# Kernel tuning notes

Hardware: AMD Instinct MI355X
Metric: run time of the kernel (lower is better)

Reference implementation:

```python
import jax, jax.numpy as jnp
import numpy as np
import math

N = 4900      # hardcoded in source (hQ[708:4900])
N1 = 708      # hardcoded group-1 size
IN, OUT, HEADS = 512, 256, 4
HD = OUT // HEADS


def _ln(x, g, b, eps):
    mu = jnp.mean(x, axis=-1, keepdims=True)
    var = jnp.var(x, axis=-1, keepdims=True)
    return (x - mu) / jnp.sqrt(var + eps) * g + b


def setup_inputs() -> dict:
    key = jax.random.key(0)
    ks = jax.random.split(key, 24)
    s = 0.05
    nrm = lambda k, shp: jax.random.normal(k, shp, jnp.float32) * s
    return {
        "feature": jax.random.normal(ks[0], (N, IN), jnp.float32),
        "adj_mat": jax.random.uniform(ks[1], (N, N), jnp.float32),
        "r": jax.random.normal(ks[2], (4, 256), jnp.float32),
        "Wq": nrm(ks[3], (IN, OUT)), "bq": jnp.zeros((OUT,), jnp.float32),
        "Wk": nrm(ks[4], (IN, OUT)), "bk": jnp.zeros((OUT,), jnp.float32),
        "Wv": nrm(ks[5], (IN, OUT)), "bv": jnp.zeros((OUT,), jnp.float32),
        "Ww": nrm(ks[6], (IN, OUT)), "bw": jnp.zeros((OUT,), jnp.float32),
        "Wr": nrm(ks[7], (256, OUT)), "br": jnp.zeros((OUT,), jnp.float32),
        "Wbeta": nrm(ks[8], (2 * OUT, OUT)), "bbeta": jnp.zeros((OUT,), jnp.float32),
        "ln1_g": jnp.ones((OUT,), jnp.float32), "ln1_b": jnp.zeros((OUT,), jnp.float32),
        "w1": nrm(ks[9], (OUT, OUT)), "b1": jnp.zeros((OUT,), jnp.float32),
        "ln2_g": jnp.ones((OUT,), jnp.float32), "ln2_b": jnp.zeros((OUT,), jnp.float32),
        "w2": nrm(ks[10], (OUT, OUT)),
        "flag": 1,
    }


def reference(feature, adj_mat, r, Wq, bq, Wk, bk, Wv, bv, Ww, bw, Wr, br,
              Wbeta, bbeta, ln1_g, ln1_b, w1, b1, ln2_g, ln2_b, w2, flag):
    H = feature @ Ww + bw                     # [N, OUT]
    rp = r @ Wr + br                          # [4, OUT]
    hQ = feature @ Wq + bq
    hK = feature @ Wk + bk
    hV = (feature @ Wv + bv).reshape(HEADS, N, HD)  # raw block reshape, as in source
    ridx = 1 if flag else 0
    # relation-modulated Q/K blocks; .view == raw reshape in the original
    hQ11 = (hQ[:N1] * rp[ridx]).reshape(HEADS, N1, HD)
    hK11 = (hK[:N1] * rp[ridx]).reshape(HEADS, N1, HD)
    hQ12 = (hQ[:N1] * rp[2]).reshape(HEADS, N1, HD)
    hQ21 = (hQ[N1:] * rp[2]).reshape(HEADS, N - N1, HD)
    hQ22 = (hQ[N1:] * rp[3]).reshape(HEADS, N - N1, HD)
    hK12 = (hK[:N1] * rp[2]).reshape(HEADS, N1, HD)
    hK21 = (hK[N1:] * rp[2]).reshape(HEADS, N - N1, HD)
    hK22 = (hK[N1:] * rp[3]).reshape(HEADS, N - N1, HD)
    a11 = jnp.einsum('hqd,hkd->hqk', hQ11, hK11)
    a12 = jnp.einsum('hqd,hkd->hqk', hQ12, hK21)
    a21 = jnp.einsum('hqd,hkd->hqk', hQ21, hK12)
    a22 = jnp.einsum('hqd,hkd->hqk', hQ22, hK22)
    alpha = jnp.concatenate([jnp.concatenate([a11, a12], axis=2),
                             jnp.concatenate([a21, a22], axis=2)], axis=1)
    alpha = alpha / math.sqrt(HEADS)          # source divides by sqrt(heads)
    alpha = alpha @ adj_mat                   # [HEADS, N, N] @ [N, N]
    # torch nn.Softmax() legacy default dim for 3D input is dim=0
    alpha = jax.nn.softmax(alpha, axis=0)
    m = alpha @ hV                            # [HEADS, N, HD]
    m = jnp.transpose(m, (1, 0, 2)).reshape(N, OUT)
    m = _ln(jax.nn.relu(m), ln1_g, ln1_b, 1e-5)
    beta = jax.nn.sigmoid(jnp.concatenate([H, m], axis=1) @ Wbeta + bbeta)
    out = beta * m + (1.0 - beta) * H
    h = jnp.tanh(_ln(out @ w1 + b1, ln2_g, ln2_b, 1e-6))
    return h @ w2
```

## Files before the change

kernel.cpp:

```cpp
#include <hip/hip_runtime.h>
#include <hip/hip_bf16.h>
#include <math.h>

#define NPOS 4900
#define NG1  708
#define NG2  4192
#define INF  512
#define OUTF 256
#define JBP  4928
#define NJT  154
#define NC   6
#define JTT  26
#define LDS_KS 36
#define PCH   2508800
#define KSPL 2112

typedef __attribute__((ext_vector_type(8))) short short8;
typedef __attribute__((ext_vector_type(16))) float f32x16;

__global__ __launch_bounds__(256) void k0_rp(
    const float* __restrict__ r, const float* __restrict__ Wr,
    const float* __restrict__ br, const int* __restrict__ flagp,
    float* __restrict__ S)
{
    __shared__ float rsh[1024];
    int t = threadIdx.x;
    for (int i = t; i < 1024; i += 256) rsh[i] = r[i];
    __syncthreads();
    float a0 = 0.f, a1 = 0.f, a2 = 0.f, a3 = 0.f;
    for (int c = 0; c < 256; ++c) {
        float w = Wr[c * 256 + t];
        a0 += rsh[c] * w;
        a1 += rsh[256 + c] * w;
        a2 += rsh[512 + c] * w;
        a3 += rsh[768 + c] * w;
    }
    float b = br[t];
    a0 += b; a1 += b; a2 += b; a3 += b;
    int ridx = (flagp[0] != 0) ? 1 : 0;
    S[t]         = ridx ? a1 : a0;
    S[256 + t]   = a2;
    S[512 + t]   = a3;
}

__global__ __launch_bounds__(256) void k1_proj(
    const float* __restrict__ feat,
    const float* __restrict__ Wq, const float* __restrict__ bq,
    const float* __restrict__ Wk, const float* __restrict__ bk,
    const float* __restrict__ Wv, const float* __restrict__ bv,
    const float* __restrict__ Ww, const float* __restrict__ bw,
    float* __restrict__ hQ, float* __restrict__ hK,
    float* __restrict__ hV, float* __restrict__ Hb)
{
    __shared__ float AT[16][68];
    __shared__ float Bs[16][132];
    int t = threadIdx.x;
    int mat = blockIdx.x >> 1;
    int n0  = (blockIdx.x & 1) * 128;
    int m0  = blockIdx.y * 64;
    const float* W; const float* bias; float* dst;
    switch (mat) {
        case 0:  W = Wq; bias = bq; dst = hQ; break;
        case 1:  W = Wk; bias = bk; dst = hK; break;
        case 2:  W = Wv; bias = bv; dst = hV; break;
        default: W = Ww; bias = bw; dst = Hb; break;
    }
    float acc[4][8];
#pragma unroll
    for (int i = 0; i < 4; ++i)
#pragma unroll
        for (int j = 0; j < 8; ++j) acc[i][j] = 0.f;
    int mg = (t >> 4) * 4, jg = (t & 15) * 8;
    int am = t & 63, ak = (t >> 6) * 4;
    int bkk = t >> 4, bn = (t & 15) * 8;
    for (int k0 = 0; k0 < INF; k0 += 16) {
        __syncthreads();
        {
            int row = m0 + am;
            float4 v = make_float4(0.f, 0.f, 0.f, 0.f);
            if (row < NPOS) v = *(const float4*)(feat + (size_t)row * INF + k0 + ak);
            AT[ak + 0][am] = v.x; AT[ak + 1][am] = v.y;
            AT[ak + 2][am] = v.z; AT[ak + 3][am] = v.w;
        }
        {
            const float* p = W + (size_t)(k0 + bkk) * OUTF + n0 + bn;
            float4 u0 = *(const float4*)p;
            float4 u1 = *(const float4*)(p + 4);
            *(float4*)&Bs[bkk][bn]     = u0;
            *(float4*)&Bs[bkk][bn + 4] = u1;
        }
        __syncthreads();
#pragma unroll
        for (int kk = 0; kk < 16; ++kk) {
            float4 a  = *(const float4*)&AT[kk][mg];
            float4 b0 = *(const float4*)&Bs[kk][jg];
            float4 b1 = *(const float4*)&Bs[kk][jg + 4];
            float av[4] = {a.x, a.y, a.z, a.w};
            float bv_[8] = {b0.x, b0.y, b0.z, b0.w, b1.x, b1.y, b1.z, b1.w};
#pragma unroll
            for (int i = 0; i < 4; ++i)
#pragma unroll
                for (int j = 0; j < 8; ++j) acc[i][j] += av[i] * bv_[j];
        }
    }
#pragma unroll
    for (int i = 0; i < 4; ++i) {
        int row = m0 + mg + i;
        if (row < NPOS) {
#pragma unroll
            for (int j = 0; j < 8; ++j) {
                int n = n0 + jg + j;
                dst[(size_t)row * OUTF + n] = acc[i][j] + bias[n];
            }
        }
    }
}

__device__ __forceinline__ void split2(float x0, float x1,
                                       unsigned& hi, unsigned& lo)
{
    unsigned u0 = __float_as_uint(x0), u1 = __float_as_uint(x1);
    unsigned h0 = u0 & 0xFFFF0000u,   h1 = u1 & 0xFFFF0000u;
    float r0 = x0 - __uint_as_float(h0);
    float r1 = x1 - __uint_as_float(h1);
    hi = (h0 >> 16) | h1;
    lo = (__float_as_uint(r0) >> 16) | (__float_as_uint(r1) & 0xFFFF0000u);
}

__device__ __forceinline__ void split1(float x, unsigned short& hi, unsigned short& lo)
{
    unsigned u = __float_as_uint(x);
    unsigned h = u & 0xFFFF0000u;
    float r = x - __uint_as_float(h);
    hi = (unsigned short)(h >> 16);
    lo = (unsigned short)(__float_as_uint(r) >> 16);
}

__device__ __forceinline__ short8 ldfrag(const unsigned short* base, int row, int kuo)
{
    const unsigned long long* p =
        (const unsigned long long*)(base + row * LDS_KS + kuo);
    union { unsigned long long q[2]; short8 s; } u;
    u.q[0] = p[0];
    u.q[1] = p[1];
    return u.s;
}

__device__ __forceinline__ short8 g16(const unsigned short* p)
{
    union { uint4 q; short8 s; } u;
    u.q = *(const uint4*)p;
    return u.s;
}

__device__ __forceinline__ short8 lds16u(const unsigned short* p)
{
    union { unsigned long long q[2]; short8 s; } u;
    u.q[0] = ((const unsigned long long*)p)[0];
    u.q[1] = ((const unsigned long long*)p)[1];
    return u.s;
}

__global__ __launch_bounds__(256) void k2_mfma(
    const float* __restrict__ hK, const float* __restrict__ adj,
    const float* __restrict__ S,
    float* __restrict__ P0, float* __restrict__ P1)
{
    __shared__ unsigned short sAh[128 * LDS_KS];
    __shared__ unsigned short sAl[128 * LDS_KS];
    __shared__ unsigned short sBh[64 * LDS_KS];
    __shared__ unsigned short sBl[64 * LDS_KS];

    int t = threadIdx.x;
    int j0 = blockIdx.x * 64;
    int h  = blockIdx.y;
    int chunk = blockIdx.z;
    int part = (chunk == 0) ? 0 : 1;
    int kbeg = (chunk <= 1) ? 0 : KSPL;
    int kend = (chunk == 0) ? NG1 : ((chunk == 2) ? NG2 : KSPL);
    int L = part ? NG2 : NG1;
    const float* kflat = hK + (part ? (size_t)NG1 * OUTF : 0);
    int rowoff = part ? NG1 : 0;
    float* Pout = chunk ? (P1 + (size_t)(chunk - 1) * PCH) : P0;

    int dd = t & 63;
    int kg = t >> 6;
    int jcol = j0 + dd;

    float sc[2][4];
#pragma unroll
    for (int g = 0; g < 2; ++g)
#pragma unroll
        for (int c = 0; c < 4; ++c)
            sc[g][c] = 0.5f * S[(g + part) * 256 + c * 64 + dd];

    f32x16 acc0, acc1;
#pragma unroll
    for (int i = 0; i < 16; ++i) { acc0[i] = 0.f; acc1[i] = 0.f; }

    int lane = t & 63;
    int half = lane >> 5;
    int ml = lane & 31;
    int arow = kg * 32 + ml;

    unsigned* uAh = (unsigned*)sAh;
    unsigned* uAl = (unsigned*)sAl;
    unsigned* uBh = (unsigned*)sBh;
    unsigned* uBl = (unsigned*)sBl;

    int ks0 = kbeg >> 5;
    int ks1 = (kend + 31) >> 5;
    for (int ks = ks0; ks < ks1; ++ks) {
        int k0 = ks * 32;
        float xa[8], xb[8];
#pragma unroll
        for (int i = 0; i < 8; ++i) {
            int kv = k0 + kg * 8 + i;
            bool okk = (kv < kend);
            xa[i] = okk ? kflat[(size_t)(h * L + kv) * 64 + dd] : 0.f;
            xb[i] = (okk && jcol < NPOS)
                        ? adj[(size_t)(rowoff + kv) * NPOS + jcol] : 0.f;
        }
        unsigned hA0[4], lA0[4], hA1[4], lA1[4], hB[4], lB[4];
#pragma unroll
        for (int i = 0; i < 8; i += 2) {
            float a0 = xa[i] * sc[0][i & 3];
            float a1 = xa[i + 1] * sc[0][(i + 1) & 3];
            split2(a0, a1, hA0[i >> 1], lA0[i >> 1]);
            float c0 = xa[i] * sc[1][i & 3];
            float c1 = xa[i + 1] * sc[1][(i + 1) & 3];
            split2(c0, c1, hA1[i >> 1], lA1[i >> 1]);
            split2(xb[i], xb[i + 1], hB[i >> 1], lB[i >> 1]);
        }
        __syncthreads();
        {
            int b0 = dd * 18 + kg * 4;
            int b1 = (64 + dd) * 18 + kg * 4;
            *(uint2*)(uAh + b0)     = make_uint2(hA0[0], hA0[1]);
            *(uint2*)(uAh + b0 + 2) = make_uint2(hA0[2], hA0[3]);
            *(uint2*)(uAl + b0)     = make_uint2(lA0[0], lA0[1]);
            *(uint2*)(uAl + b0 + 2) = make_uint2(lA0[2], lA0[3]);
            *(uint2*)(uAh + b1)     = make_uint2(hA1[0], hA1[1]);
            *(uint2*)(uAh + b1 + 2) = make_uint2(hA1[2], hA1[3]);
            *(uint2*)(uAl + b1)     = make_uint2(lA1[0], lA1[1]);
            *(uint2*)(uAl + b1 + 2) = make_uint2(lA1[2], lA1[3]);
            *(uint2*)(uBh + b0)     = make_uint2(hB[0], hB[1]);
            *(uint2*)(uBh + b0 + 2) = make_uint2(hB[2], hB[3]);
            *(uint2*)(uBl + b0)     = make_uint2(lB[0], lB[1]);
            *(uint2*)(uBl + b0 + 2) = make_uint2(lB[2], lB[3]);
        }
        __syncthreads();
#pragma unroll
        for (int kq = 0; kq < 2; ++kq) {
            int kuo = kq * 16 + half * 8;
            short8 aH = ldfrag(sAh, arow, kuo);
            short8 aL = ldfrag(sAl, arow, kuo);
            short8 b0H = ldfrag(sBh, ml, kuo);
            short8 b0L = ldfrag(sBl, ml, kuo);
            short8 b1H = ldfrag(sBh, 32 + ml, kuo);
            short8 b1L = ldfrag(sBl, 32 + ml, kuo);
            acc0 = __builtin_amdgcn_mfma_f32_32x32x16_bf16(aH, b0H, acc0, 0, 0, 0);
            acc0 = __builtin_amdgcn_mfma_f32_32x32x16_bf16(aH, b0L, acc0, 0, 0, 0);
            acc0 = __builtin_amdgcn_mfma_f32_32x32x16_bf16(aL, b0H, acc0, 0, 0, 0);
            acc1 = __builtin_amdgcn_mfma_f32_32x32x16_bf16(aH, b1H, acc1, 0, 0, 0);
            acc1 = __builtin_amdgcn_mfma_f32_32x32x16_bf16(aH, b1L, acc1, 0, 0, 0);
            acc1 = __builtin_amdgcn_mfma_f32_32x32x16_bf16(aL, b1H, acc1, 0, 0, 0);
        }
    }

    int col0 = j0 + ml;
    int col1 = j0 + 32 + ml;
#pragma unroll
    for (int reg = 0; reg < 16; ++reg) {
        int m = kg * 32 + (reg & 3) + 8 * (reg >> 2) + 4 * half;
        int g = m >> 6, ddm = m & 63;
        size_t rb = (size_t)((h * 2 + g) * 64 + ddm) * NPOS;
        Pout[rb + col0] = acc0[reg];
        if (col1 < NPOS) Pout[rb + col1] = acc1[reg];
    }
}

__global__ __launch_bounds__(256) void k2_reduce(
    const float* __restrict__ P0, const float* __restrict__ P1,
    unsigned short* __restrict__ Bhi, unsigned short* __restrict__ Blo)
{
    int t = threadIdx.x;
    int j = blockIdx.x * 256 + t;
    if (j >= JBP) return;
    int p = blockIdx.y;
    int g = p >> 2, h = p & 3;
    int kg = blockIdx.z;
    int k0 = kg * 16;
    int rowb = (h * 2 + g) * 64;

    unsigned short hi[16], lo[16];
    if (j < NPOS) {
        if (k0 < 64) {
#pragma unroll
            for (int i = 0; i < 16; ++i) {
                float v = P0[(size_t)(rowb + k0 + i) * NPOS + j];
                split1(v, hi[i], lo[i]);
            }
        } else {
#pragma unroll
            for (int i = 0; i < 16; ++i) {
                size_t off = (size_t)(rowb + (k0 - 64) + i) * NPOS + j;
                float v = P1[off] + P1[off + PCH];
                split1(v, hi[i], lo[i]);
            }
        }
    } else {
#pragma unroll
        for (int i = 0; i < 16; ++i) { hi[i] = 0; lo[i] = 0; }
    }
    size_t base = ((size_t)p * JBP + j) * 128 + k0;
    union { unsigned short us[16]; uint4 v[2]; } uh, ul;
#pragma unroll
    for (int i = 0; i < 16; ++i) { uh.us[i] = hi[i]; ul.us[i] = lo[i]; }
    *(uint4*)(Bhi + base)     = uh.v[0];
    *(uint4*)(Bhi + base + 8) = uh.v[1];
    *(uint4*)(Blo + base)     = ul.v[0];
    *(uint4*)(Blo + base + 8) = ul.v[1];
}

__global__ __launch_bounds__(256) void qsplit(
    const float* __restrict__ hQ, const float* __restrict__ S,
    unsigned short* __restrict__ Qh, unsigned short* __restrict__ Ql)
{
    int t = threadIdx.x;
    int row = blockIdx.x * 2 + (t >> 7);
    int k = t & 127;
    int g, h, ql, Lg, vbase;
    if (row < 3072) { g = 0; h = row / 768; ql = row - h * 768; Lg = NG1; vbase = 0; }
    else {
        int rr = row - 3072;
        g = 1; h = rr / 4224; ql = rr - h * 4224; Lg = NG2; vbase = NG1 * OUTF;
    }
    int d = k & 63, p = k >> 6;
    float v = 0.f;
    if (ql < Lg)
        v = hQ[vbase + (size_t)(h * Lg + ql) * 64 + d] *
            S[(g + p) * 256 + (ql & 3) * 64 + d];
    unsigned short hi, lo;
    split1(v, hi, lo);
    Qh[(size_t)row * 128 + k] = hi;
    Ql[(size_t)row * 128 + k] = lo;
}

__global__ __launch_bounds__(256) void vtsplit(
    const float* __restrict__ hV,
    unsigned short* __restrict__ VtH, unsigned short* __restrict__ VtL)
{
    __shared__ float ls[128 * 65];
    int t = threadIdx.x;
    int j0 = blockIdx.x * 128;
    int h  = blockIdx.y;
#pragma unroll
    for (int i = 0; i < 32; ++i) {
        int idx = t + i * 256;
        int j = idx >> 6, d = idx & 63;
        float v = 0.f;
        int jg = j0 + j;
        if (jg < NPOS) v = hV[(size_t)(h * NPOS + jg) * 64 + d];
        ls[j * 65 + d] = v;
    }
    __syncthreads();
    int d = t >> 2, jseg = (t & 3) * 32;
#pragma unroll
    for (int i = 0; i < 32; ++i) {
        int j = jseg + i;
        int jg = j0 + j;
        if (jg < JBP) {
            unsigned short hi, lo;
            split1(ls[j * 65 + d], hi, lo);
            VtH[(size_t)(h * 64 + d) * JBP + jg] = hi;
            VtL[(size_t)(h * 64 + d) * JBP + jg] = lo;
        }
    }
}

__global__ __launch_bounds__(256, 2) void k3f_attn(
    const unsigned short* __restrict__ Qh, const unsigned short* __restrict__ Ql,
    const unsigned short* __restrict__ Bhi, const unsigned short* __restrict__ Blo,
    const unsigned short* __restrict__ VtH, const unsigned short* __restrict__ VtL,
    float* __restrict__ mpart)
{
    __shared__ __align__(16) char smem[35328];
    float* La = (float*)smem;
    unsigned short* Aa = (unsigned short*)(smem + 16896);

    int t = threadIdx.x;
    int w = t >> 6, lane = t & 63;
    int half = lane >> 5, ml = lane & 31;
    int h = w;

    int x = blockIdx.x;
    int c = blockIdx.y;
    int g = (x < 23) ? 0 : 1;
    int tile = g ? (x - 23) : x;
    int Lg = g ? NG2 : NG1;
    int posbase = g ? NG1 : 0;
    int qbase = g ? 3072 : 0;
    int hstr = g ? 4224 : 768;
    int q0 = tile * 32;

    const unsigned short* qrowH = Qh + (size_t)(qbase + h * hstr + q0 + ml) * 128 + half * 8;
    const unsigned short* qrowL = Ql + (size_t)(qbase + h * hstr + q0 + ml) * 128 + half * 8;
    short8 qfH[8], qfL[8];
#pragma unroll
    for (int kc = 0; kc < 8; ++kc) {
        qfH[kc] = g16(qrowH + kc * 16);
        qfL[kc] = g16(qrowL + kc * 16);
    }

    const unsigned short* bHb = Bhi + ((size_t)(g * 4 + h) * JBP + ml) * 128 + half * 8;
    const unsigned short* bLb = Blo + ((size_t)(g * 4 + h) * JBP + ml) * 128 + half * 8;
    size_t vro = (size_t)(h * 64 + ml) * JBP;
    const unsigned short* vH0 = VtH + vro;
    const unsigned short* vL0 = VtL + vro;
    const unsigned short* vH1 = VtH + vro + (size_t)32 * JBP;
    const unsigned short* vL1 = VtL + vro + (size_t)32 * JBP;

    f32x16 pv[2];
#pragma unroll
    for (int n = 0; n < 2; ++n)
#pragma unroll
        for (int r = 0; r < 16; ++r) pv[n][r] = 0.f;

    int spos = t >> 3, sj4 = (t & 7) * 4;

    int jt0 = c * JTT, jt1 = jt0 + JTT;
    if (jt1 > NJT) jt1 = NJT;

    for (int jt = jt0; jt < jt1; ++jt) {
        int j0 = jt * 32;
        const unsigned short* bH = bHb + (size_t)j0 * 128;
        const unsigned short* bL = bLb + (size_t)j0 * 128;

        short8 bb[8];
#pragma unroll
        for (int kc = 0; kc < 8; ++kc) bb[kc] = g16(bH + kc * 16);
        int joA = j0 + half * 8;
        int joB = j0 + 16 + half * 8;
        short8 vh0a = g16(vH0 + joA);
        short8 vh1a = g16(vH1 + joA);
        short8 vh0b = g16(vH0 + joB);
        short8 vh1b = g16(vH1 + joB);

        f32x16 qka, qkb;
#pragma unroll
        for (int r = 0; r < 16; ++r) { qka[r] = 0.f; qkb[r] = 0.f; }
#pragma unroll
        for (int kc = 0; kc < 8; kc += 2) {
            qka = __builtin_amdgcn_mfma_f32_32x32x16_bf16(bb[kc], qfH[kc], qka, 0, 0, 0);
            qka = __builtin_amdgcn_mfma_f32_32x32x16_bf16(bb[kc], qfL[kc], qka, 0, 0, 0);
            qkb = __builtin_amdgcn_mfma_f32_32x32x16_bf16(bb[kc + 1], qfH[kc + 1], qkb, 0, 0, 0);
            qkb = __builtin_amdgcn_mfma_f32_32x32x16_bf16(bb[kc + 1], qfL[kc + 1], qkb, 0, 0, 0);
        }
#pragma unroll
        for (int kc = 0; kc < 8; ++kc) bb[kc] = g16(bL + kc * 16);
#pragma unroll
        for (int kc = 0; kc < 8; kc += 2) {
            qka = __builtin_amdgcn_mfma_f32_32x32x16_bf16(bb[kc], qfH[kc], qka, 0, 0, 0);
            qkb = __builtin_amdgcn_mfma_f32_32x32x16_bf16(bb[kc + 1], qfH[kc + 1], qkb, 0, 0, 0);
        }

#pragma unroll
        for (int r = 0; r < 16; ++r) {
            int jrow = (r & 3) + 8 * (r >> 2) + 4 * half;
            La[(w * 32 + jrow) * 33 + ml] = qka[r] + qkb[r];
        }
        __syncthreads();
        {
            unsigned short hi_[4][4], lo_[4][4];
#pragma unroll
            for (int jj = 0; jj < 4; ++jj) {
                int j = sj4 + jj;
                float v0 = La[(0 * 32 + j) * 33 + spos];
                float v1 = La[(1 * 32 + j) * 33 + spos];
                float v2 = La[(2 * 32 + j) * 33 + spos];
                float v3 = La[(3 * 32 + j) * 33 + spos];
                float mx = fmaxf(fmaxf(v0, v1), fmaxf(v2, v3));
                float e0 = __expf(v0 - mx), e1 = __expf(v1 - mx);
                float e2 = __expf(v2 - mx), e3 = __expf(v3 - mx);
                float inv = 1.0f / (e0 + e1 + e2 + e3);
                split1(e0 * inv, hi_[0][jj], lo_[0][jj]);
                split1(e1 * inv, hi_[1][jj], lo_[1][jj]);
                split1(e2 * inv, hi_[2][jj], lo_[2][jj]);
                split1(e3 * inv, hi_[3][jj], lo_[3][jj]);
            }
#pragma unroll
            for (int hh = 0; hh < 4; ++hh) {
                unsigned long long Hw =
                    (unsigned long long)hi_[hh][0] |
                    ((unsigned long long)hi_[hh][1] << 16) |
                    ((unsigned long long)hi_[hh][2] << 32) |
                    ((unsigned long long)hi_[hh][3] << 48);
                unsigned long long Lw =
                    (unsigned long long)lo_[hh][0] |
                    ((unsigned long long)lo_[hh][1] << 16) |
                    ((unsigned long long)lo_[hh][2] << 32) |
                    ((unsigned long long)lo_[hh][3] << 48);
                *(unsigned long long*)&Aa[((hh * 2 + 0) * 32 + spos) * 36 + sj4] = Hw;
                *(unsigned long long*)&Aa[((hh * 2 + 1) * 32 + spos) * 36 + sj4] = Lw;
            }
        }
        __syncthreads();
        const unsigned short* aBH = Aa + (size_t)((w * 2 + 0) * 32 + ml) * 36 + half * 8;
        const unsigned short* aBL = Aa + (size_t)((w * 2 + 1) * 32 + ml) * 36 + half * 8;
        short8 w0La = g16(vL0 + joA);
        short8 w1La = g16(vL1 + joA);
        short8 w0Lb = g16(vL0 + joB);
        short8 w1Lb = g16(vL1 + joB);
#pragma unroll
        for (int ck = 0; ck < 2; ++ck) {
            short8 paH = lds16u(aBH + ck * 16);
            short8 paL = lds16u(aBL + ck * 16);
            short8 w0H = ck ? vh0b : vh0a;
            short8 w1H = ck ? vh1b : vh1a;
            short8 w0L = ck ? w0Lb : w0La;
            short8 w1L = ck ? w1Lb : w1La;
            pv[0] = __builtin_amdgcn_mfma_f32_32x32x16_bf16(w0H, paH, pv[0], 0, 0, 0);
            pv[0] = __builtin_amdgcn_mfma_f32_32x32x16_bf16(w0H, paL, pv[0], 0, 0, 0);
            pv[0] = __builtin_amdgcn_mfma_f32_32x32x16_bf16(w0L, paH, pv[0], 0, 0, 0);
            pv[1] = __builtin_amdgcn_mfma_f32_32x32x16_bf16(w1H, paH, pv[1], 0, 0, 0);
            pv[1] = __builtin_amdgcn_mfma_f32_32x32x16_bf16(w1H, paL, pv[1], 0, 0, 0);
            pv[1] = __builtin_amdgcn_mfma_f32_32x32x16_bf16(w1L, paH, pv[1], 0, 0, 0);
        }
    }

    __syncthreads();
    float* scr = (float*)smem + w * 2112;
#pragma unroll
    for (int nt = 0; nt < 2; ++nt)
#pragma unroll
        for (int r = 0; r < 16; ++r) {
            int drow = (r & 3) + 8 * (r >> 2) + 4 * half;
            scr[ml * 66 + nt * 32 + drow] = pv[nt][r];
        }
    float* mpc = mpart + (size_t)c * NPOS * OUTF;
#pragma unroll 4
    for (int i = 0; i < 32; ++i) {
        int pg = q0 + i;
        if (pg < Lg)
            mpc[(size_t)(posbase + pg) * OUTF + h * 64 + lane] = scr[i * 66 + lane];
    }
}

__global__ __launch_bounds__(256) void e1_relu_ln(
    const float* __restrict__ mpart, const float* __restrict__ Hb,
    const float* __restrict__ g1, const float* __restrict__ b1,
    float* __restrict__ cc)
{
    int w = threadIdx.x >> 6, lane = threadIdx.x & 63;
    int row = blockIdx.x * 4 + w;
    int c = lane * 4;
    const size_t CST = (size_t)NPOS * OUTF;
    float4 x0 = *(const float4*)(mpart + (size_t)row * OUTF + c);
#pragma unroll
    for (int k = 1; k < NC; ++k) {
        float4 a = *(const float4*)(mpart + k * CST + (size_t)row * OUTF + c);
        x0.x += a.x; x0.y += a.y; x0.z += a.z; x0.w += a.w;
    }
    float x[4] = { fmaxf(x0.x, 0.f), fmaxf(x0.y, 0.f),
                   fmaxf(x0.z, 0.f), fmaxf(x0.w, 0.f) };
    float s = x[0] + x[1] + x[2] + x[3];
#pragma unroll
    for (int m = 32; m > 0; m >>= 1) s += __shfl_xor(s, m, 64);
    float mu = s * (1.0f / 256.0f);
    float vs = 0.f;
#pragma unroll
    for (int i = 0; i < 4; ++i) { float d = x[i] - mu; vs += d * d; }
#pragma unroll
    for (int m = 32; m > 0; m >>= 1) vs += __shfl_xor(vs, m, 64);
    float rs = rsqrtf(vs * (1.0f / 256.0f) + 1e-5f);
    float4 y;
    y.x = (x[0] - mu) * rs * g1[c + 0] + b1[c + 0];
    y.y = (x[1] - mu) * rs * g1[c + 1] + b1[c + 1];
    y.z = (x[2] - mu) * rs * g1[c + 2] + b1[c + 2];
    y.w = (x[3] - mu) * rs * g1[c + 3] + b1[c + 3];
    *(float4*)(cc + (size_t)row * INF + OUTF + c) = y;
    float4 hh = *(const float4*)(Hb + (size_t)row * OUTF + c);
    *(float4*)(cc + (size_t)row * INF + c) = hh;
}

__global__ __launch_bounds__(256) void e2_beta(
    const float* __restrict__ cc, const float* __restrict__ Wb,
    const float* __restrict__ bb, float* __restrict__ outb)
{
    __shared__ float AT[16][68];
    __shared__ float Bs[16][132];
    int t = threadIdx.x;
    int n0 = blockIdx.x * 128;
    int m0 = blockIdx.y * 64;
    float acc[4][8];
#pragma unroll
    for (int i = 0; i < 4; ++i)
#pragma unroll
        for (int j = 0; j < 8; ++j) acc[i][j] = 0.f;
    int mg = (t >> 4) * 4, jg = (t & 15) * 8;
    int am = t & 63, ak = (t >> 6) * 4;
    int bkk = t >> 4, bn = (t & 15) * 8;
    for (int k0 = 0; k0 < INF; k0 += 16) {
        __syncthreads();
        {
            int row = m0 + am;
            float4 v = make_float4(0.f, 0.f, 0.f, 0.f);
            if (row < NPOS) v = *(const float4*)(cc + (size_t)row * INF + k0 + ak);
            AT[ak + 0][am] = v.x; AT[ak + 1][am] = v.y;
            AT[ak + 2][am] = v.z; AT[ak + 3][am] = v.w;
        }
        {
            const float* p = Wb + (size_t)(k0 + bkk) * OUTF + n0 + bn;
            float4 u0 = *(const float4*)p;
            float4 u1 = *(const float4*)(p + 4);
            *(float4*)&Bs[bkk][bn]     = u0;
            *(float4*)&Bs[bkk][bn + 4] = u1;
        }
        __syncthreads();
#pragma unroll
        for (int kk = 0; kk < 16; ++kk) {
            float4 a  = *(const float4*)&AT[kk][mg];
            float4 b0 = *(const float4*)&Bs[kk][jg];
            float4 b1 = *(const float4*)&Bs[kk][jg + 4];
            float av[4] = {a.x, a.y, a.z, a.w};
            float bv_[8] = {b0.x, b0.y, b0.z, b0.w, b1.x, b1.y, b1.z, b1.w};
#pragma unroll
            for (int i = 0; i < 4; ++i)
#pragma unroll
                for (int j = 0; j < 8; ++j) acc[i][j] += av[i] * bv_[j];
        }
    }
#pragma unroll
    for (int i = 0; i < 4; ++i) {
        int row = m0 + mg + i;
        if (row < NPOS) {
#pragma unroll
            for (int j = 0; j < 8; ++j) {
                int n = n0 + jg + j;
                float x = acc[i][j] + bb[n];
                float sg = 1.0f / (1.0f + __expf(-x));
                float m1v = cc[(size_t)row * INF + OUTF + n];
                float Hv  = cc[(size_t)row * INF + n];
                outb[(size_t)row * OUTF + n] = sg * m1v + (1.0f - sg) * Hv;
            }
        }
    }
}

__global__ __launch_bounds__(256) void e3_w1_ln2(
    const float* __restrict__ outb, const float* __restrict__ w1,
    const float* __restrict__ b1v, const float* __restrict__ g2,
    const float* __restrict__ b2v, float* __restrict__ h2o)
{
    __shared__ float As[16][260];
    __shared__ float Bs[16][260];
    __shared__ float red[16][17];
    int t = threadIdx.x;
    int m0 = blockIdx.x * 16;
    {
        int rr = t >> 4, c4 = (t & 15) * 4;
        int row = m0 + rr;
#pragma unroll
        for (int i = 0; i < 4; ++i) {
            int c = c4 + i * 64;
            float4 x = make_float4(0.f, 0.f, 0.f, 0.f);
            if (row < NPOS) x = *(const float4*)(outb + (size_t)row * OUTF + c);
            *(float4*)&As[rr][c] = x;
        }
    }
    int q = t & 15, dg = (t >> 4) * 16;
    float acc[16];
#pragma unroll
    for (int i = 0; i < 16; ++i) acc[i] = 0.f;
    for (int k0 = 0; k0 < 256; k0 += 16) {
        __syncthreads();
        {
            int kk = t >> 4, n16 = (t & 15) * 16;
#pragma unroll
            for (int i = 0; i < 4; ++i) {
                float4 x = *(const float4*)(w1 + (size_t)(k0 + kk) * OUTF + n16 + i * 4);
                *(float4*)&Bs[kk][n16 + i * 4] = x;
            }
        }
        __syncthreads();
#pragma unroll
        for (int kk = 0; kk < 16; ++kk) {
            float a = As[q][k0 + kk];
#pragma unroll
            for (int i = 0; i < 16; i += 4) {
                float4 b = *(const float4*)&Bs[kk][dg + i];
                acc[i + 0] += a * b.x; acc[i + 1] += a * b.y;
                acc[i + 2] += a * b.z; acc[i + 3] += a * b.w;
            }
        }
    }
    float x[16];
#pragma unroll
    for (int i = 0; i < 16; ++i) x[i] = acc[i] + b1v[dg + i];
    float ps = 0.f;
#pragma unroll
    for (int i = 0; i < 16; ++i) ps += x[i];
    __syncthreads();
    red[t >> 4][q] = ps;
    __syncthreads();
    float s = 0.f;
#pragma unroll
    for (int i = 0; i < 16; ++i) s += red[i][q];
    float mu = s * (1.0f / 256.0f);
    float pvv = 0.f;
#pragma unroll
    for (int i = 0; i < 16; ++i) { float d = x[i] - mu; pvv += d * d; }
    __syncthreads();
    red[t >> 4][q] = pvv;
    __syncthreads();
    float v = 0.f;
#pragma unroll
    for (int i = 0; i < 16; ++i) v += red[i][q];
    float rs = rsqrtf(v * (1.0f / 256.0f) + 1e-6f);
    int row = m0 + q;
    if (row < NPOS) {
#pragma unroll
        for (int i = 0; i < 16; ++i) {
            int n = dg + i;
            h2o[(size_t)row * OUTF + n] = tanhf((x[i] - mu) * rs * g2[n] + b2v[n]);
        }
    }
}

__global__ __launch_bounds__(256) void e4_final(
    const float* __restrict__ h2in, const float* __restrict__ w2,
    float* __restrict__ outp)
{
    __shared__ float AT[16][68];
    __shared__ float Bs[16][132];
    int t = threadIdx.x;
    int n0 = blockIdx.x * 128;
    int m0 = blockIdx.y * 64;
    float acc[4][8];
#pragma unroll
    for (int i = 0; i < 4; ++i)
#pragma unroll
        for (int j = 0; j < 8; ++j) acc[i][j] = 0.f;
    int mg = (t >> 4) * 4, jg = (t & 15) * 8;
    int am = t & 63, ak = (t >> 6) * 4;
    int bkk = t >> 4, bn = (t & 15) * 8;
    for (int k0 = 0; k0 < 256; k0 += 16) {
        __syncthreads();
        {
            int row = m0 + am;
            float4 v = make_float4(0.f, 0.f, 0.f, 0.f);
            if (row < NPOS) v = *(const float4*)(h2in + (size_t)row * OUTF + k0 + ak);
            AT[ak + 0][am] = v.x; AT[ak + 1][am] = v.y;
            AT[ak + 2][am] = v.z; AT[ak + 3][am] = v.w;
        }
        {
            const float* p = w2 + (size_t)(k0 + bkk) * OUTF + n0 + bn;
            float4 u0 = *(const float4*)p;
            float4 u1 = *(const float4*)(p + 4);
            *(float4*)&Bs[bkk][bn]     = u0;
            *(float4*)&Bs[bkk][bn + 4] = u1;
        }
        __syncthreads();
#pragma unroll
        for (int kk = 0; kk < 16; ++kk) {
            float4 a  = *(const float4*)&AT[kk][mg];
            float4 b0 = *(const float4*)&Bs[kk][jg];
            float4 b1 = *(const float4*)&Bs[kk][jg + 4];
            float av[4] = {a.x, a.y, a.z, a.w};
            float bv_[8] = {b0.x, b0.y, b0.z, b0.w, b1.x, b1.y, b1.z, b1.w};
#pragma unroll
            for (int i = 0; i < 4; ++i)
#pragma unroll
                for (int j = 0; j < 8; ++j) acc[i][j] += av[i] * bv_[j];
        }
    }
#pragma unroll
    for (int i = 0; i < 4; ++i) {
        int row = m0 + mg + i;
        if (row < NPOS) {
#pragma unroll
            for (int j = 0; j < 8; ++j) {
                outp[(size_t)row * OUTF + n0 + jg + j] = acc[i][j];
            }
        }
    }
}

extern "C" void kernel_launch(void* const* d_in, const int* in_sizes, int n_in,
                              void* d_out, int out_size, void* d_ws, size_t ws_size,
                              hipStream_t stream)
{
    const float* feature = (const float*)d_in[0];
    const float* adj   = (const float*)d_in[1];
    const float* r     = (const float*)d_in[2];
    const float* Wq    = (const float*)d_in[3];
    const float* bq    = (const float*)d_in[4];
    const float* Wk    = (const float*)d_in[5];
    const float* bk    = (const float*)d_in[6];
    const float* Wv    = (const float*)d_in[7];
    const float* bv    = (const float*)d_in[8];
    const float* Ww    = (const float*)d_in[9];
    const float* bw    = (const float*)d_in[10];
    const float* Wr    = (const float*)d_in[11];
    const float* br    = (const float*)d_in[12];
    const float* Wbeta = (const float*)d_in[13];
    const float* bbeta = (const float*)d_in[14];
    const float* ln1g  = (const float*)d_in[15];
    const float* ln1b  = (const float*)d_in[16];
    const float* w1    = (const float*)d_in[17];
    const float* b1    = (const float*)d_in[18];
    const float* ln2g  = (const float*)d_in[19];
    const float* ln2b  = (const float*)d_in[20];
    const float* w2    = (const float*)d_in[21];
    const int*   flag  = (const int*)d_in[22];
    float* out = (float*)d_out;

    char* ws = (char*)d_ws;
    unsigned short* Qh    = (unsigned short*)(ws + 0);
    unsigned short* Qlo   = (unsigned short*)(ws + 5111808);
    unsigned short* VtH   = (unsigned short*)(ws + 10223616);
    unsigned short* VtL   = (unsigned short*)(ws + 12746752);
    float*          Hb    = (float*)(ws + 15269888);
    float*          P0    = (float*)(ws + 20287488);
    float*          P1    = (float*)(ws + 30322688);
    float*          mpart = (float*)(ws + 20287488);
    unsigned short* Bhi   = (unsigned short*)(ws + 50393088);
    unsigned short* Blo   = (unsigned short*)(ws + 60485632);
    float*          hK    = (float*)(ws + 50393088);
    float*          hQ    = (float*)(ws + 60485632);
    float*          hV    = (float*)(ws + 65503232);
    float*          cc    = (float*)(ws + 0);
    float*          outb  = (float*)(ws + 10223616);
    float*          hh2   = (float*)(ws + 20287488);
    float*          S     = (float*)(ws + 70578176);

    k0_rp<<<1, 256, 0, stream>>>(r, Wr, br, flag, S);
    k1_proj<<<dim3(8, 77), 256, 0, stream>>>(feature, Wq, bq, Wk, bk, Wv, bv, Ww, bw,
                                             hQ, hK, hV, Hb);
    qsplit<<<9984, 256, 0, stream>>>(hQ, S, Qh, Qlo);
    vtsplit<<<dim3(39, 4), 256, 0, stream>>>(hV, VtH, VtL);
    k2_mfma<<<dim3(77, 4, 3), 256, 0, stream>>>(hK, adj, S, P0, P1);
    k2_reduce<<<dim3(20, 8, 8), 256, 0, stream>>>(P0, P1, Bhi, Blo);
    k3f_attn<<<dim3(154, NC), 256, 0, stream>>>(Qh, Qlo, Bhi, Blo, VtH, VtL, mpart);
    e1_relu_ln<<<1225, 256, 0, stream>>>(mpart, Hb, ln1g, ln1b, cc);
    e2_beta<<<dim3(2, 77), 256, 0, stream>>>(cc, Wbeta, bbeta, outb);
    e3_w1_ln2<<<307, 256, 0, stream>>>(outb, w1, b1, ln2g, ln2b, hh2);
    e4_final<<<dim3(2, 77), 256, 0, stream>>>(hh2, w2, out);
}
```

Baseline: 859.1 us.

## Store B and Vt in MFMA-fragment order and prefetch next B-hi tile

The producer kernels now write the adjacency-product B operand and the transposed V split into a fragment-major layout, so each lane's 16-byte load in the attention kernel is contiguous across the wavefront. The attention loop also loads the next tile's B-hi fragments early, letting them overlap with the current tile's MFMAs, and issues the V loads together. The aim is to cut strided, uncoalesced global loads and hide load latency, at the cost of more live registers under the 2-waves launch bound.

```diff
diff --git a/kernel.cpp b/kernel.cpp
--- a/kernel.cpp
+++ b/kernel.cpp
@@ -313,14 +313,15 @@
 #pragma unroll
         for (int i = 0; i < 16; ++i) { hi[i] = 0; lo[i] = 0; }
     }
-    size_t base = ((size_t)p * JBP + j) * 128 + k0;
+    int jt = j >> 5, mlr = j & 31;
+    size_t fb = (((size_t)p * NJT + jt) * 8 + kg) * 512;
     union { unsigned short us[16]; uint4 v[2]; } uh, ul;
 #pragma unroll
     for (int i = 0; i < 16; ++i) { uh.us[i] = hi[i]; ul.us[i] = lo[i]; }
-    *(uint4*)(Bhi + base)     = uh.v[0];
-    *(uint4*)(Bhi + base + 8) = uh.v[1];
-    *(uint4*)(Blo + base)     = ul.v[0];
-    *(uint4*)(Blo + base + 8) = ul.v[1];
+    *(uint4*)(Bhi + fb + (size_t)mlr * 8)       = uh.v[0];
+    *(uint4*)(Bhi + fb + 256 + (size_t)mlr * 8) = uh.v[1];
+    *(uint4*)(Blo + fb + (size_t)mlr * 8)       = ul.v[0];
+    *(uint4*)(Blo + fb + 256 + (size_t)mlr * 8) = ul.v[1];
 }
 
 __global__ __launch_bounds__(256) void qsplit(
@@ -365,16 +366,27 @@
         ls[j * 65 + d] = v;
     }
     __syncthreads();
-    int d = t >> 2, jseg = (t & 3) * 32;
-#pragma unroll
-    for (int i = 0; i < 32; ++i) {
-        int j = jseg + i;
-        int jg = j0 + j;
-        if (jg < JBP) {
-            unsigned short hi, lo;
-            split1(ls[j * 65 + d], hi, lo);
-            VtH[(size_t)(h * 64 + d) * JBP + jg] = hi;
-            VtL[(size_t)(h * 64 + d) * JBP + jg] = lo;
+    int jtbase = j0 >> 5;
+#pragma unroll
+    for (int it = 0; it < 4; ++it) {
+        int chunk = t + it * 256;
+        int jtl = chunk >> 8;
+        int r = chunk & 255;
+        int ck = r >> 7;
+        int r2 = r & 127;
+        int nt = r2 >> 6;
+        int l = r2 & 63;
+        int jt = jtbase + jtl;
+        if (jt < NJT) {
+            int d = nt * 32 + (l & 31);
+            int jloc = jtl * 32 + ck * 16 + (l >> 5) * 8;
+            union { unsigned short us[8]; uint4 v; } uh, ul;
+#pragma unroll
+            for (int i = 0; i < 8; ++i)
+                split1(ls[(jloc + i) * 65 + d], uh.us[i], ul.us[i]);
+            size_t fb = ((((size_t)h * NJT + jt) * 2 + ck) * 2 + nt) * 512 + (size_t)l * 8;
+            *(uint4*)(VtH + fb) = uh.v;
+            *(uint4*)(VtL + fb) = ul.v;
         }
     }
 }
@@ -413,13 +425,10 @@
         qfL[kc] = g16(qrowL + kc * 16);
     }
 
-    const unsigned short* bHb = Bhi + ((size_t)(g * 4 + h) * JBP + ml) * 128 + half * 8;
-    const unsigned short* bLb = Blo + ((size_t)(g * 4 + h) * JBP + ml) * 128 + half * 8;
-    size_t vro = (size_t)(h * 64 + ml) * JBP;
-    const unsigned short* vH0 = VtH + vro;
-    const unsigned short* vL0 = VtL + vro;
-    const unsigned short* vH1 = VtH + vro + (size_t)32 * JBP;
-    const unsigned short* vL1 = VtL + vro + (size_t)32 * JBP;
+    const unsigned short* bfH = Bhi + (size_t)(g * 4 + h) * NJT * 4096 + (size_t)lane * 8;
+    const unsigned short* bfL = Blo + (size_t)(g * 4 + h) * NJT * 4096 + (size_t)lane * 8;
+    const unsigned short* vfH = VtH + (size_t)h * NJT * 2048 + (size_t)lane * 8;
+    const unsigned short* vfL = VtL + (size_t)h * NJT * 2048 + (size_t)lane * 8;
 
     f32x16 pv[2];
 #pragma unroll
@@ -432,37 +441,45 @@
     int jt0 = c * JTT, jt1 = jt0 + JTT;
     if (jt1 > NJT) jt1 = NJT;
 
+    short8 bbH[8];
+#pragma unroll
+    for (int kc = 0; kc < 8; ++kc)
+        bbH[kc] = g16(bfH + (size_t)jt0 * 4096 + kc * 512);
+
     for (int jt = jt0; jt < jt1; ++jt) {
-        int j0 = jt * 32;
-        const unsigned short* bH = bHb + (size_t)j0 * 128;
-        const unsigned short* bL = bLb + (size_t)j0 * 128;
-
-        short8 bb[8];
-#pragma unroll
-        for (int kc = 0; kc < 8; ++kc) bb[kc] = g16(bH + kc * 16);
-        int joA = j0 + half * 8;
-        int joB = j0 + 16 + half * 8;
-        short8 vh0a = g16(vH0 + joA);
-        short8 vh1a = g16(vH1 + joA);
-        short8 vh0b = g16(vH0 + joB);
-        short8 vh1b = g16(vH1 + joB);
+        size_t jo = (size_t)jt * 4096;
+        int jn = (jt + 1 < jt1) ? jt + 1 : jt;
+        size_t jno = (size_t)jn * 4096;
+
+        short8 bbL[8];
+#pragma unroll
+        for (int kc = 0; kc < 8; ++kc) bbL[kc] = g16(bfL + jo + kc * 512);
 
         f32x16 qka, qkb;
 #pragma unroll
         for (int r = 0; r < 16; ++r) { qka[r] = 0.f; qkb[r] = 0.f; }
 #pragma unroll
         for (int kc = 0; kc < 8; kc += 2) {
-            qka = __builtin_amdgcn_mfma_f32_32x32x16_bf16(bb[kc], qfH[kc], qka, 0, 0, 0);
-            qka = __builtin_amdgcn_mfma_f32_32x32x16_bf16(bb[kc], qfL[kc], qka, 0, 0, 0);
-            qkb = __builtin_amdgcn_mfma_f32_32x32x16_bf16(bb[kc + 1], qfH[kc + 1], qkb, 0, 0, 0);
-            qkb = __builtin_amdgcn_mfma_f32_32x32x16_bf16(bb[kc + 1], qfL[kc + 1], qkb, 0, 0, 0);
-        }
-#pragma unroll
-        for (int kc = 0; kc < 8; ++kc) bb[kc] = g16(bL + kc * 16);
+            qka = __builtin_amdgcn_mfma_f32_32x32x16_bf16(bbH[kc], qfH[kc], qka, 0, 0, 0);
+            qka = __builtin_amdgcn_mfma_f32_32x32x16_bf16(bbH[kc], qfL[kc], qka, 0, 0, 0);
+            qkb = __builtin_amdgcn_mfma_f32_32x32x16_bf16(bbH[kc + 1], qfH[kc + 1], qkb, 0, 0, 0);
+            qkb = __builtin_amdgcn_mfma_f32_32x32x16_bf16(bbH[kc + 1], qfL[kc + 1], qkb, 0, 0, 0);
+        }
+#pragma unroll
+        for (int kc = 0; kc < 8; ++kc) bbH[kc] = g16(bfH + jno + kc * 512);
+
 #pragma unroll
         for (int kc = 0; kc < 8; kc += 2) {
-            qka = __builtin_amdgcn_mfma_f32_32x32x16_bf16(bb[kc], qfH[kc], qka, 0, 0, 0);
-            qkb = __builtin_amdgcn_mfma_f32_32x32x16_bf16(bb[kc + 1], qfH[kc + 1], qkb, 0, 0, 0);
+            qka = __builtin_amdgcn_mfma_f32_32x32x16_bf16(bbL[kc], qfH[kc], qka, 0, 0, 0);
+            qkb = __builtin_amdgcn_mfma_f32_32x32x16_bf16(bbL[kc + 1], qfH[kc + 1], qkb, 0, 0, 0);
+        }
+
+        short8 vt[8];
+        size_t vo = (size_t)jt * 2048;
+#pragma unroll
+        for (int q2 = 0; q2 < 4; ++q2) {
+            vt[q2]     = g16(vfH + vo + q2 * 512);
+            vt[4 + q2] = g16(vfL + vo + q2 * 512);
         }
 
 #pragma unroll
@@ -508,18 +525,14 @@
         __syncthreads();
         const unsigned short* aBH = Aa + (size_t)((w * 2 + 0) * 32 + ml) * 36 + half * 8;
         const unsigned short* aBL = Aa + (size_t)((w * 2 + 1) * 32 + ml) * 36 + half * 8;
-        short8 w0La = g16(vL0 + joA);
-        short8 w1La = g16(vL1 + joA);
-        short8 w0Lb = g16(vL0 + joB);
-        short8 w1Lb = g16(vL1 + joB);
 #pragma unroll
         for (int ck = 0; ck < 2; ++ck) {
             short8 paH = lds16u(aBH + ck * 16);
             short8 paL = lds16u(aBL + ck * 16);
-            short8 w0H = ck ? vh0b : vh0a;
-            short8 w1H = ck ? vh1b : vh1a;
-            short8 w0L = ck ? w0Lb : w0La;
-            short8 w1L = ck ? w1Lb : w1La;
+            short8 w0H = vt[ck * 2 + 0];
+            short8 w1H = vt[ck * 2 + 1];
+            short8 w0L = vt[4 + ck * 2 + 0];
+            short8 w1L = vt[4 + ck * 2 + 1];
             pv[0] = __builtin_amdgcn_mfma_f32_32x32x16_bf16(w0H, paH, pv[0], 0, 0, 0);
             pv[0] = __builtin_amdgcn_mfma_f32_32x32x16_bf16(w0H, paL, pv[0], 0, 0, 0);
             pv[0] = __builtin_amdgcn_mfma_f32_32x32x16_bf16(w0L, paH, pv[0], 0, 0, 0);
```

Result: faster. 699.6 us (-18.6%).
